# Kernel tuning notes

Measured on AMD Instinct MI355X. Metric: run time of the kernel, lower is better.

Reference implementation:

```python
import jax, jax.numpy as jnp
import numpy as np

B, S, N = 1, 128, 256
C_IN, C_H, C_OUT = 256, 32, 128
EPS = 1e-5


def setup_inputs() -> dict:
    key = jax.random.key(0)
    k_m, k_wa, k_wb, k_wo = jax.random.split(key, 4)
    m = jax.random.normal(k_m, (B, S, N, C_IN), dtype=jnp.float32)
    mask = jnp.ones((B, S, N), dtype=jnp.float32)
    gamma = jnp.ones((C_IN,), dtype=jnp.float32)
    beta = jnp.zeros((C_IN,), dtype=jnp.float32)
    # nn.Linear weights are (out, in)
    Wa = jax.random.normal(k_wa, (C_H, C_IN), dtype=jnp.float32) / np.sqrt(C_IN).astype(np.float32)
    Wb = jax.random.normal(k_wb, (C_H, C_IN), dtype=jnp.float32) / np.sqrt(C_IN).astype(np.float32)
    # proj_o is final_init (zeros) in the source; use small random weights so the
    # baseline output is non-trivial for correctness checking.
    Wo = jax.random.normal(k_wo, (C_OUT, C_H * C_H), dtype=jnp.float32) / np.sqrt(C_H * C_H).astype(np.float32)
    bo = jnp.zeros((C_OUT,), dtype=jnp.float32)
    return {"m": m, "mask": mask, "gamma": gamma, "beta": beta,
            "Wa": Wa, "Wb": Wb, "Wo": Wo, "bo": bo}


def reference(m, mask, gamma, beta, Wa, Wb, Wo, bo):
    # LayerNorm over c_in
    mu = jnp.mean(m, axis=-1, keepdims=True)
    var = jnp.mean((m - mu) ** 2, axis=-1, keepdims=True)
    mn = (m - mu) * jax.lax.rsqrt(var + EPS) * gamma + beta  # (B,S,N,c_in)

    mk = mask[..., None]  # (B,S,N,1)
    a = jnp.einsum('bsni,hi->bsnh', mn, Wa) * mk  # (B,S,N,c_h)
    b = jnp.einsum('bsni,hi->bsnh', mn, Wb) * mk  # (B,S,N,c_h)

    # pairwise mask count over S, clamped to >= 1
    num_mask = jnp.clip(jnp.einsum('bsi,bsj->bij', mask, mask), 1.0, None)  # (B,N,N)

    # outer-product mean over the sequence dim
    z = jnp.einsum('bsic,bsjd->bijcd', a, b)  # (B,N,N,c_h,c_h)
    z = z.reshape(z.shape[0], z.shape[1], z.shape[2], C_H * C_H)
    z = z / num_mask[..., None]

    return jnp.einsum('bijk,ok->bijo', z, Wo) + bo  # (B,N,N,c_out)
```

## Files before the change

### kernel.cpp

```cpp
#include <hip/hip_runtime.h>

#define S_DIM 128
#define N_DIM 256
#define CIN   256
#define CH    32
#define COUT  128

typedef __attribute__((ext_vector_type(8))) short bf16x8;
typedef __attribute__((ext_vector_type(4))) float f32x4;

__device__ __forceinline__ unsigned short f2bf(float f) {
  union { float f; unsigned int u; } v; v.f = f;
  unsigned int u = v.u;
  return (unsigned short)((u + 0x7FFFu + ((u >> 16) & 1u)) >> 16);
}

__global__ __launch_bounds__(256) void lnp_prep_kernel(
    const float* __restrict__ m, const float* __restrict__ mask,
    const float* __restrict__ gamma, const float* __restrict__ beta,
    const float* __restrict__ Wa, const float* __restrict__ Wb,
    const float* __restrict__ Wo,
    float* __restrict__ rnm, unsigned short* __restrict__ wo2,
    unsigned short* __restrict__ a_t, unsigned short* __restrict__ b_t) {
  const int b = blockIdx.x, t = threadIdx.x;
  if (b < 1024) {
    __shared__ __align__(16) unsigned short mn[32][264];
    __shared__ __align__(16) unsigned short wabs[64 * 256];
    const int i = b & 255, s0 = (b >> 8) * 32;
    const int w = t >> 6, l = t & 63, lq = l >> 4, lr = l & 15;

    #pragma unroll
    for (int it = 0; it < 8; it++) {
      const int gi = it * 256 + t;
      const int r = gi >> 5, g = gi & 31;
      const float* src = (r < 32) ? (Wa + r * 256 + g * 8)
                                  : (Wb + (r - 32) * 256 + g * 8);
      const int gp = (g & 16) | ((g ^ (r & 15)) & 15);
      unsigned short* dst = &wabs[r * 256 + gp * 8];
      const float4 v0 = *(const float4*)(src);
      const float4 v1 = *(const float4*)(src + 4);
      dst[0] = f2bf(v0.x); dst[1] = f2bf(v0.y); dst[2] = f2bf(v0.z); dst[3] = f2bf(v0.w);
      dst[4] = f2bf(v1.x); dst[5] = f2bf(v1.y); dst[6] = f2bf(v1.z); dst[7] = f2bf(v1.w);
    }

    const float4 g4 = *(const float4*)(gamma + l * 4);
    const float4 b4 = *(const float4*)(beta + l * 4);

    for (int rr = 0; rr < 8; rr++) {
      const int r = w * 8 + rr;
      const int s = s0 + r;
      const float4 v = *(const float4*)(m + ((size_t)(s * N_DIM + i)) * CIN + l * 4);
      float sum = v.x + v.y + v.z + v.w;
      float sq  = v.x * v.x + v.y * v.y + v.z * v.z + v.w * v.w;
      #pragma unroll
      for (int off = 32; off > 0; off >>= 1) {
        sum += __shfl_down(sum, off);
        sq  += __shfl_down(sq, off);
      }
      sum = __shfl(sum, 0); sq = __shfl(sq, 0);
      const float mu = sum * (1.0f / CIN);
      const float var = fmaxf(sq * (1.0f / CIN) - mu * mu, 0.0f);
      const float rs = rsqrtf(var + 1e-5f);
      const float mk = mask[s * N_DIM + i];
      ushort4 p;
      p.x = f2bf(((v.x - mu) * rs * g4.x + b4.x) * mk);
      p.y = f2bf(((v.y - mu) * rs * g4.y + b4.y) * mk);
      p.z = f2bf(((v.z - mu) * rs * g4.z + b4.z) * mk);
      p.w = f2bf(((v.w - mu) * rs * g4.w + b4.w) * mk);
      *(ushort4*)(&mn[r][l * 4]) = p;
    }
    __syncthreads();

    const int wm = w & 1;
    const int n2 = w >> 1;
    f32x4 acc0 = {0.f, 0.f, 0.f, 0.f}, acc1 = {0.f, 0.f, 0.f, 0.f};
    #pragma unroll
    for (int ks = 0; ks < 8; ks++) {
      const int k0 = ks * 32 + lq * 8;
      const int g = ks * 4 + lq;
      const int gp = (g & 16) | ((g ^ lr) & 15);
      const bf16x8 af = *(const bf16x8*)(&mn[wm * 16 + lr][k0]);
      const bf16x8 bf0 = *(const bf16x8*)(&wabs[(n2 * 32 + lr) * 256 + gp * 8]);
      const bf16x8 bf1 = *(const bf16x8*)(&wabs[(n2 * 32 + 16 + lr) * 256 + gp * 8]);
      acc0 = __builtin_amdgcn_mfma_f32_16x16x32_bf16(af, bf0, acc0, 0, 0, 0);
      acc1 = __builtin_amdgcn_mfma_f32_16x16x32_bf16(af, bf1, acc1, 0, 0, 0);
    }

    unsigned short* dst = (n2 == 0) ? a_t : b_t;
    const int scol = s0 + wm * 16 + lq * 4;
    ushort4 q0, q1;
    q0.x = f2bf(acc0[0]); q0.y = f2bf(acc0[1]); q0.z = f2bf(acc0[2]); q0.w = f2bf(acc0[3]);
    q1.x = f2bf(acc1[0]); q1.y = f2bf(acc1[1]); q1.z = f2bf(acc1[2]); q1.w = f2bf(acc1[3]);
    *(ushort4*)(dst + ((size_t)(i * CH + lr)) * S_DIM + scol) = q0;
    *(ushort4*)(dst + ((size_t)(i * CH + 16 + lr)) * S_DIM + scol) = q1;
  } else if (b < 1152) {
    const int r = b - 1024;
    #pragma unroll
    for (int q = 0; q < 4; q++) {
      const int f = r * 1024 + q * 256 + t;
      const int e = f & 7, l = (f >> 3) & 63, kk = (f >> 9) & 31, ot = f >> 14;
      const int kp = kk * 32 + (l >> 4) * 8 + e;
      const int c = kp & 31, d = kp >> 5;
      const int o = ot * 16 + (l & 15);
      wo2[f] = f2bf(Wo[o * 1024 + c * 32 + d]);
    }
  } else {
    const int i = b - 1152;
    float acc = 0.f;
    #pragma unroll 8
    for (int s = 0; s < S_DIM; s++)
      acc += mask[s * N_DIM + i] * mask[s * N_DIM + t];
    acc = fmaxf(acc, 1.0f);
    rnm[i * N_DIM + t] = 1.0f / acc;
  }
}

__global__ __launch_bounds__(1024, 4) void fused_kernel(
    const unsigned short* __restrict__ a_t, const unsigned short* __restrict__ b_t,
    const unsigned short* __restrict__ wo2, const float* __restrict__ rnm,
    const float* __restrict__ bo, float* __restrict__ out) {
  extern __shared__ __align__(16) unsigned short smem[];
  unsigned short* sA = smem;
  unsigned short* sB = smem + 32768;
  unsigned short* sZ = smem;

  const int t = threadIdx.x, w = t >> 6, l = t & 63;
  const int lq = l >> 4, lr = l & 15;
  const int bx = blockIdx.x, by = blockIdx.y;

  const unsigned short* srcA = a_t + (size_t)bx * 32768;
  const unsigned short* srcB = b_t + (size_t)by * 32768;
  #pragma unroll
  for (int it = 0; it < 4; it++) {
    const int idx = it * 1024 + t;
    const int r = idx >> 4, g = idx & 15;
    const int dst = r * 128 + ((g ^ (r & 15)) * 8);
    *(bf16x8*)(&sA[dst]) = *(const bf16x8*)(srcA + idx * 8);
    *(bf16x8*)(&sB[dst]) = *(const bf16x8*)(srcB + idx * 8);
  }
  __syncthreads();

  const int wy = (w >> 2) * 64, wx = (w & 3) * 64;
  f32x4 acc[4][4];
  #pragma unroll
  for (int a = 0; a < 4; a++)
    #pragma unroll
    for (int c = 0; c < 4; c++) acc[a][c] = (f32x4){0.f, 0.f, 0.f, 0.f};

  #pragma unroll
  for (int ks = 0; ks < 4; ks++) {
    const int g0 = ks * 4 + lq;
    bf16x8 afr[4], bfr[4];
    #pragma unroll
    for (int a = 0; a < 4; a++) {
      const int ra = wy + a * 16 + lr;
      afr[a] = *(const bf16x8*)(&sA[ra * 128 + ((g0 ^ (ra & 15)) * 8)]);
      const int rb = wx + a * 16 + lr;
      bfr[a] = *(const bf16x8*)(&sB[rb * 128 + ((g0 ^ (rb & 15)) * 8)]);
    }
    #pragma unroll
    for (int a = 0; a < 4; a++)
      #pragma unroll
      for (int c = 0; c < 4; c++)
        acc[a][c] = __builtin_amdgcn_mfma_f32_16x16x32_bf16(afr[a], bfr[c], acc[a][c], 0, 0, 0);
  }
  __syncthreads();

  #pragma unroll
  for (int a = 0; a < 4; a++) {
    #pragma unroll
    for (int c = 0; c < 4; c++) {
      const int zrb = wy + a * 16 + lq * 4;
      const int zc  = wx + c * 16 + lr;
      const int pair = (zrb >> 5) * 8 + (zc >> 5);
      const int off = (zc & 31) * 32 + (zrb & 31);
      const int g = off >> 3;
      const int gp = (g & ~7) | ((g ^ (g >> 3) ^ pair) & 7);
      ushort4 q;
      q.x = f2bf(acc[a][c][0]); q.y = f2bf(acc[a][c][1]);
      q.z = f2bf(acc[a][c][2]); q.w = f2bf(acc[a][c][3]);
      *(ushort4*)(&sZ[pair * 1024 + gp * 8 + (off & 7)]) = q;
    }
  }
  __syncthreads();

  const int ot = w >> 1, wm2 = w & 1;
  const int p0 = wm2 * 32 + lr, p1 = p0 + 16;
  const unsigned short* wbase = wo2 + (size_t)ot * 16384 + (size_t)l * 8;
  f32x4 oa[2][2];
  oa[0][0] = oa[0][1] = oa[1][0] = oa[1][1] = (f32x4){0.f, 0.f, 0.f, 0.f};
  #pragma unroll 4
  for (int kk = 0; kk < 32; kk++) {
    const int g = kk * 4 + lq;
    const int gp0 = (g & ~7) | ((g ^ (g >> 3) ^ p0) & 7);
    const int gp1 = (g & ~7) | ((g ^ (g >> 3) ^ p1) & 7);
    const bf16x8 wf = *(const bf16x8*)(wbase + kk * 512);
    const bf16x8 z0 = *(const bf16x8*)(&sZ[p0 * 1024 + gp0 * 8]);
    const bf16x8 z1 = *(const bf16x8*)(&sZ[p1 * 1024 + gp1 * 8]);
    oa[0][kk & 1] = __builtin_amdgcn_mfma_f32_16x16x32_bf16(z0, wf, oa[0][kk & 1], 0, 0, 0);
    oa[1][kk & 1] = __builtin_amdgcn_mfma_f32_16x16x32_bf16(z1, wf, oa[1][kk & 1], 0, 0, 0);
  }

  const int o = ot * 16 + lr;
  const float bov = bo[o];
  #pragma unroll
  for (int f = 0; f < 2; f++) {
    #pragma unroll
    for (int r = 0; r < 4; r++) {
      const int pair = wm2 * 32 + f * 16 + lq * 4 + r;
      const int ii = bx * 8 + (pair >> 3);
      const int jj = by * 8 + (pair & 7);
      const float sc = rnm[ii * N_DIM + jj];
      out[((size_t)(ii * N_DIM + jj)) * COUT + o] =
          (oa[f][0][r] + oa[f][1][r]) * sc + bov;
    }
  }
}

extern "C" void kernel_launch(void* const* d_in, const int* in_sizes, int n_in,
                              void* d_out, int out_size, void* d_ws, size_t ws_size,
                              hipStream_t stream) {
  const float* m     = (const float*)d_in[0];
  const float* mask  = (const float*)d_in[1];
  const float* gamma = (const float*)d_in[2];
  const float* beta  = (const float*)d_in[3];
  const float* Wa    = (const float*)d_in[4];
  const float* Wb    = (const float*)d_in[5];
  const float* Wo    = (const float*)d_in[6];
  const float* bo    = (const float*)d_in[7];
  float* out = (float*)d_out;

  char* ws = (char*)d_ws;
  float*          rnm = (float*)(ws);
  unsigned short* wo2 = (unsigned short*)(ws + 262144);
  unsigned short* a_t = (unsigned short*)(ws + 524288);
  unsigned short* b_t = (unsigned short*)(ws + 2621440);

  hipFuncSetAttribute((const void*)fused_kernel,
                      hipFuncAttributeMaxDynamicSharedMemorySize, 131072);

  lnp_prep_kernel<<<1408, 256, 0, stream>>>(m, mask, gamma, beta, Wa, Wb, Wo,
                                            rnm, wo2, a_t, b_t);
  fused_kernel<<<dim3(32, 32), 1024, 131072, stream>>>(a_t, b_t, wo2, rnm, bo, out);
}
```

Baseline: 147.7 us.

## Split LayerNorm and projection into separate kernels, remap fused grid

The LayerNorm now runs in its own pass over contiguous rows, so each block reads m with coalesced row loads instead of strided per-i gathers, and writes normalized bf16 activations to a workspace buffer. A new projection kernel reads that buffer and multiplies by weights pre-converted to bf16 in global memory, replacing the per-block conversion of Wa/Wb into shared memory. The fused kernel moves to a 1D grid with a remapped block order, which is meant to improve L2 reuse of the a/b tiles. The cost is an extra kernel launch and an extra round trip of the normalized activations (about 16MB) through global memory.

```diff
diff --git a/kernel.cpp b/kernel.cpp
--- a/kernel.cpp
+++ b/kernel.cpp
@@ -15,43 +15,28 @@
   return (unsigned short)((u + 0x7FFFu + ((u >> 16) & 1u)) >> 16);
 }
 
-__global__ __launch_bounds__(256) void lnp_prep_kernel(
+__global__ __launch_bounds__(256) void k0_ln_prep(
     const float* __restrict__ m, const float* __restrict__ mask,
     const float* __restrict__ gamma, const float* __restrict__ beta,
     const float* __restrict__ Wa, const float* __restrict__ Wb,
     const float* __restrict__ Wo,
-    float* __restrict__ rnm, unsigned short* __restrict__ wo2,
-    unsigned short* __restrict__ a_t, unsigned short* __restrict__ b_t) {
+    float* __restrict__ rnm, unsigned short* __restrict__ wab_bf,
+    unsigned short* __restrict__ wo2, unsigned short* __restrict__ mn_g) {
   const int b = blockIdx.x, t = threadIdx.x;
-  if (b < 1024) {
-    __shared__ __align__(16) unsigned short mn[32][264];
-    __shared__ __align__(16) unsigned short wabs[64 * 256];
-    const int i = b & 255, s0 = (b >> 8) * 32;
-    const int w = t >> 6, l = t & 63, lq = l >> 4, lr = l & 15;
-
-    #pragma unroll
-    for (int it = 0; it < 8; it++) {
-      const int gi = it * 256 + t;
-      const int r = gi >> 5, g = gi & 31;
-      const float* src = (r < 32) ? (Wa + r * 256 + g * 8)
-                                  : (Wb + (r - 32) * 256 + g * 8);
-      const int gp = (g & 16) | ((g ^ (r & 15)) & 15);
-      unsigned short* dst = &wabs[r * 256 + gp * 8];
-      const float4 v0 = *(const float4*)(src);
-      const float4 v1 = *(const float4*)(src + 4);
-      dst[0] = f2bf(v0.x); dst[1] = f2bf(v0.y); dst[2] = f2bf(v0.z); dst[3] = f2bf(v0.w);
-      dst[4] = f2bf(v1.x); dst[5] = f2bf(v1.y); dst[6] = f2bf(v1.z); dst[7] = f2bf(v1.w);
-    }
-
+  if (b < 2048) {
+    const int w = t >> 6, l = t & 63;
+    const int rbase = b * 16 + w * 4;
     const float4 g4 = *(const float4*)(gamma + l * 4);
     const float4 b4 = *(const float4*)(beta + l * 4);
-
-    for (int rr = 0; rr < 8; rr++) {
-      const int r = w * 8 + rr;
-      const int s = s0 + r;
-      const float4 v = *(const float4*)(m + ((size_t)(s * N_DIM + i)) * CIN + l * 4);
-      float sum = v.x + v.y + v.z + v.w;
-      float sq  = v.x * v.x + v.y * v.y + v.z * v.z + v.w * v.w;
+    float4 v[4];
+    #pragma unroll
+    for (int rr = 0; rr < 4; rr++)
+      v[rr] = *(const float4*)(m + (size_t)(rbase + rr) * CIN + l * 4);
+    #pragma unroll
+    for (int rr = 0; rr < 4; rr++) {
+      float sum = v[rr].x + v[rr].y + v[rr].z + v[rr].w;
+      float sq  = v[rr].x * v[rr].x + v[rr].y * v[rr].y +
+                  v[rr].z * v[rr].z + v[rr].w * v[rr].w;
       #pragma unroll
       for (int off = 32; off > 0; off >>= 1) {
         sum += __shfl_down(sum, off);
@@ -61,40 +46,20 @@
       const float mu = sum * (1.0f / CIN);
       const float var = fmaxf(sq * (1.0f / CIN) - mu * mu, 0.0f);
       const float rs = rsqrtf(var + 1e-5f);
-      const float mk = mask[s * N_DIM + i];
+      const float mk = mask[rbase + rr];
       ushort4 p;
-      p.x = f2bf(((v.x - mu) * rs * g4.x + b4.x) * mk);
-      p.y = f2bf(((v.y - mu) * rs * g4.y + b4.y) * mk);
-      p.z = f2bf(((v.z - mu) * rs * g4.z + b4.z) * mk);
-      p.w = f2bf(((v.w - mu) * rs * g4.w + b4.w) * mk);
-      *(ushort4*)(&mn[r][l * 4]) = p;
-    }
-    __syncthreads();
-
-    const int wm = w & 1;
-    const int n2 = w >> 1;
-    f32x4 acc0 = {0.f, 0.f, 0.f, 0.f}, acc1 = {0.f, 0.f, 0.f, 0.f};
-    #pragma unroll
-    for (int ks = 0; ks < 8; ks++) {
-      const int k0 = ks * 32 + lq * 8;
-      const int g = ks * 4 + lq;
-      const int gp = (g & 16) | ((g ^ lr) & 15);
-      const bf16x8 af = *(const bf16x8*)(&mn[wm * 16 + lr][k0]);
-      const bf16x8 bf0 = *(const bf16x8*)(&wabs[(n2 * 32 + lr) * 256 + gp * 8]);
-      const bf16x8 bf1 = *(const bf16x8*)(&wabs[(n2 * 32 + 16 + lr) * 256 + gp * 8]);
-      acc0 = __builtin_amdgcn_mfma_f32_16x16x32_bf16(af, bf0, acc0, 0, 0, 0);
-      acc1 = __builtin_amdgcn_mfma_f32_16x16x32_bf16(af, bf1, acc1, 0, 0, 0);
-    }
-
-    unsigned short* dst = (n2 == 0) ? a_t : b_t;
-    const int scol = s0 + wm * 16 + lq * 4;
-    ushort4 q0, q1;
-    q0.x = f2bf(acc0[0]); q0.y = f2bf(acc0[1]); q0.z = f2bf(acc0[2]); q0.w = f2bf(acc0[3]);
-    q1.x = f2bf(acc1[0]); q1.y = f2bf(acc1[1]); q1.z = f2bf(acc1[2]); q1.w = f2bf(acc1[3]);
-    *(ushort4*)(dst + ((size_t)(i * CH + lr)) * S_DIM + scol) = q0;
-    *(ushort4*)(dst + ((size_t)(i * CH + 16 + lr)) * S_DIM + scol) = q1;
-  } else if (b < 1152) {
-    const int r = b - 1024;
+      p.x = f2bf(((v[rr].x - mu) * rs * g4.x + b4.x) * mk);
+      p.y = f2bf(((v[rr].y - mu) * rs * g4.y + b4.y) * mk);
+      p.z = f2bf(((v[rr].z - mu) * rs * g4.z + b4.z) * mk);
+      p.w = f2bf(((v[rr].w - mu) * rs * g4.w + b4.w) * mk);
+      *(ushort4*)(mn_g + (size_t)(rbase + rr) * CIN + l * 4) = p;
+    }
+  } else if (b < 2112) {
+    const int r = b - 2048;
+    const float* src = (r < 32) ? (Wa + r * CIN) : (Wb + (r - 32) * CIN);
+    wab_bf[r * CIN + t] = f2bf(src[t]);
+  } else if (b < 2240) {
+    const int r = b - 2112;
     #pragma unroll
     for (int q = 0; q < 4; q++) {
       const int f = r * 1024 + q * 256 + t;
@@ -105,7 +70,7 @@
       wo2[f] = f2bf(Wo[o * 1024 + c * 32 + d]);
     }
   } else {
-    const int i = b - 1152;
+    const int i = b - 2240;
     float acc = 0.f;
     #pragma unroll 8
     for (int s = 0; s < S_DIM; s++)
@@ -113,6 +78,47 @@
     acc = fmaxf(acc, 1.0f);
     rnm[i * N_DIM + t] = 1.0f / acc;
   }
+}
+
+__global__ __launch_bounds__(256) void proj_kernel(
+    const unsigned short* __restrict__ mn_g,
+    const unsigned short* __restrict__ wab_bf,
+    unsigned short* __restrict__ a_t, unsigned short* __restrict__ b_t) {
+  __shared__ __align__(16) unsigned short mn[32][264];
+  const int i = blockIdx.x;
+  const int s0 = blockIdx.y * 32;
+  const int t = threadIdx.x, w = t >> 6, l = t & 63;
+  const int lq = l >> 4, lr = l & 15;
+
+  #pragma unroll
+  for (int rr = 0; rr < 8; rr++) {
+    const int r = w * 8 + rr;
+    const size_t rid = (size_t)(s0 + r) * N_DIM + i;
+    *(ushort4*)(&mn[r][l * 4]) = *(const ushort4*)(mn_g + rid * CIN + l * 4);
+  }
+  __syncthreads();
+
+  const int wm = w & 1;
+  const int n2 = w >> 1;
+  f32x4 acc0 = {0.f, 0.f, 0.f, 0.f}, acc1 = {0.f, 0.f, 0.f, 0.f};
+  #pragma unroll
+  for (int ks = 0; ks < 8; ks++) {
+    const int k0 = ks * 32 + lq * 8;
+    const bf16x8 af = *(const bf16x8*)(&mn[wm * 16 + lr][k0]);
+    const unsigned short* wrow = wab_bf + (n2 * 32 + lr) * CIN + k0;
+    const bf16x8 bf0 = *(const bf16x8*)(wrow);
+    const bf16x8 bf1 = *(const bf16x8*)(wrow + 16 * CIN);
+    acc0 = __builtin_amdgcn_mfma_f32_16x16x32_bf16(af, bf0, acc0, 0, 0, 0);
+    acc1 = __builtin_amdgcn_mfma_f32_16x16x32_bf16(af, bf1, acc1, 0, 0, 0);
+  }
+
+  unsigned short* dst = (n2 == 0) ? a_t : b_t;
+  const int scol = s0 + wm * 16 + lq * 4;
+  ushort4 q0, q1;
+  q0.x = f2bf(acc0[0]); q0.y = f2bf(acc0[1]); q0.z = f2bf(acc0[2]); q0.w = f2bf(acc0[3]);
+  q1.x = f2bf(acc1[0]); q1.y = f2bf(acc1[1]); q1.z = f2bf(acc1[2]); q1.w = f2bf(acc1[3]);
+  *(ushort4*)(dst + ((size_t)(i * CH + lr)) * S_DIM + scol) = q0;
+  *(ushort4*)(dst + ((size_t)(i * CH + 16 + lr)) * S_DIM + scol) = q1;
 }
 
 __global__ __launch_bounds__(1024, 4) void fused_kernel(
@@ -126,7 +132,10 @@
 
   const int t = threadIdx.x, w = t >> 6, l = t & 63;
   const int lq = l >> 4, lr = l & 15;
-  const int bx = blockIdx.x, by = blockIdx.y;
+  const int lin = blockIdx.x;
+  const int li = lin >> 3;
+  const int by = ((lin & 7) << 2) | (li >> 5);
+  const int bx = li & 31;
 
   const unsigned short* srcA = a_t + (size_t)bx * 32768;
   const unsigned short* srcB = b_t + (size_t)by * 32768;
@@ -231,15 +240,18 @@
   float* out = (float*)d_out;
 
   char* ws = (char*)d_ws;
-  float*          rnm = (float*)(ws);
-  unsigned short* wo2 = (unsigned short*)(ws + 262144);
-  unsigned short* a_t = (unsigned short*)(ws + 524288);
-  unsigned short* b_t = (unsigned short*)(ws + 2621440);
+  float*          rnm    = (float*)(ws);
+  unsigned short* wo2    = (unsigned short*)(ws + 262144);
+  unsigned short* wab_bf = (unsigned short*)(ws + 524288);
+  unsigned short* a_t    = (unsigned short*)(ws + 557056);
+  unsigned short* b_t    = (unsigned short*)(ws + 2654208);
+  unsigned short* mn_g   = (unsigned short*)(ws + 4751360);
 
   hipFuncSetAttribute((const void*)fused_kernel,
                       hipFuncAttributeMaxDynamicSharedMemorySize, 131072);
 
-  lnp_prep_kernel<<<1408, 256, 0, stream>>>(m, mask, gamma, beta, Wa, Wb, Wo,
-                                            rnm, wo2, a_t, b_t);
-  fused_kernel<<<dim3(32, 32), 1024, 131072, stream>>>(a_t, b_t, wo2, rnm, bo, out);
-}
+  k0_ln_prep<<<2496, 256, 0, stream>>>(m, mask, gamma, beta, Wa, Wb, Wo,
+                                       rnm, wab_bf, wo2, mn_g);
+  proj_kernel<<<dim3(256, 4), 256, 0, stream>>>(mn_g, wab_bf, a_t, b_t);
+  fused_kernel<<<1024, 1024, 131072, stream>>>(a_t, b_t, wo2, rnm, bo, out);
+}
```

Result: slower. 155.7 us (+5.5%).

## Reassign output-projection warp tiling and use packed bf16 conversion

Applied to the files above, without the earlier changes.

The Wo projection stage is retiled so each warp handles 16 pairs against two 16-wide output tiles, reading one Z fragment from LDS and two Wo fragments from global memory, where before it read two Z fragments and one Wo fragment. This trades LDS reads for global/L2 weight reads. The fp32-to-bf16 conversion of the outer-product accumulators also moves from manual bit arithmetic to the packed __float22bfloat162_rn intrinsic, which may map to a hardware packed-convert instruction.

```diff
diff --git a/kernel.cpp b/kernel.cpp
--- a/kernel.cpp
+++ b/kernel.cpp
@@ -1,4 +1,5 @@
 #include <hip/hip_runtime.h>
+#include <hip/hip_bf16.h>
 
 #define S_DIM 128
 #define N_DIM 256
@@ -13,6 +14,13 @@
   union { float f; unsigned int u; } v; v.f = f;
   unsigned int u = v.u;
   return (unsigned short)((u + 0x7FFFu + ((u >> 16) & 1u)) >> 16);
+}
+
+__device__ __forceinline__ unsigned int pk2(float x, float y) {
+  float2 f2; f2.x = x; f2.y = y;
+  __hip_bfloat162 h = __float22bfloat162_rn(f2);
+  union { __hip_bfloat162 h; unsigned int u; } c; c.h = h;
+  return c.u;
 }
 
 __global__ __launch_bounds__(256) void lnp_prep_kernel(
@@ -176,38 +184,38 @@
       const int off = (zc & 31) * 32 + (zrb & 31);
       const int g = off >> 3;
       const int gp = (g & ~7) | ((g ^ (g >> 3) ^ pair) & 7);
-      ushort4 q;
-      q.x = f2bf(acc[a][c][0]); q.y = f2bf(acc[a][c][1]);
-      q.z = f2bf(acc[a][c][2]); q.w = f2bf(acc[a][c][3]);
-      *(ushort4*)(&sZ[pair * 1024 + gp * 8 + (off & 7)]) = q;
+      uint2 q;
+      q.x = pk2(acc[a][c][0], acc[a][c][1]);
+      q.y = pk2(acc[a][c][2], acc[a][c][3]);
+      *(uint2*)(&sZ[pair * 1024 + gp * 8 + (off & 7)]) = q;
     }
   }
   __syncthreads();
 
-  const int ot = w >> 1, wm2 = w & 1;
-  const int p0 = wm2 * 32 + lr, p1 = p0 + 16;
-  const unsigned short* wbase = wo2 + (size_t)ot * 16384 + (size_t)l * 8;
+  const int pg = w & 3, og = w >> 2;
+  const int p = pg * 16 + lr;
+  const unsigned short* wbase0 = wo2 + (size_t)(og * 2) * 16384 + (size_t)l * 8;
+  const unsigned short* wbase1 = wbase0 + 16384;
   f32x4 oa[2][2];
   oa[0][0] = oa[0][1] = oa[1][0] = oa[1][1] = (f32x4){0.f, 0.f, 0.f, 0.f};
   #pragma unroll 4
   for (int kk = 0; kk < 32; kk++) {
     const int g = kk * 4 + lq;
-    const int gp0 = (g & ~7) | ((g ^ (g >> 3) ^ p0) & 7);
-    const int gp1 = (g & ~7) | ((g ^ (g >> 3) ^ p1) & 7);
-    const bf16x8 wf = *(const bf16x8*)(wbase + kk * 512);
-    const bf16x8 z0 = *(const bf16x8*)(&sZ[p0 * 1024 + gp0 * 8]);
-    const bf16x8 z1 = *(const bf16x8*)(&sZ[p1 * 1024 + gp1 * 8]);
-    oa[0][kk & 1] = __builtin_amdgcn_mfma_f32_16x16x32_bf16(z0, wf, oa[0][kk & 1], 0, 0, 0);
-    oa[1][kk & 1] = __builtin_amdgcn_mfma_f32_16x16x32_bf16(z1, wf, oa[1][kk & 1], 0, 0, 0);
-  }
-
-  const int o = ot * 16 + lr;
-  const float bov = bo[o];
+    const int gp = (g & ~7) | ((g ^ (g >> 3) ^ p) & 7);
+    const bf16x8 zf = *(const bf16x8*)(&sZ[p * 1024 + gp * 8]);
+    const bf16x8 w0 = *(const bf16x8*)(wbase0 + kk * 512);
+    const bf16x8 w1 = *(const bf16x8*)(wbase1 + kk * 512);
+    oa[0][kk & 1] = __builtin_amdgcn_mfma_f32_16x16x32_bf16(zf, w0, oa[0][kk & 1], 0, 0, 0);
+    oa[1][kk & 1] = __builtin_amdgcn_mfma_f32_16x16x32_bf16(zf, w1, oa[1][kk & 1], 0, 0, 0);
+  }
+
   #pragma unroll
   for (int f = 0; f < 2; f++) {
+    const int o = (og * 2 + f) * 16 + lr;
+    const float bov = bo[o];
     #pragma unroll
     for (int r = 0; r < 4; r++) {
-      const int pair = wm2 * 32 + f * 16 + lq * 4 + r;
+      const int pair = pg * 16 + lq * 4 + r;
       const int ii = bx * 8 + (pair >> 3);
       const int jj = by * 8 + (pair & 7);
       const float sc = rnm[ii * N_DIM + jj];
```

Result: slower. 157.2 us (+6.5%).
